# Optimization experiments

Measured on AMD Instinct MI355X. Metric: run time of the kernel, lower is better.

## Reference

```python
import jax, jax.numpy as jnp
import numpy as np

EPS = 1e-08
MARGIN = 0.5
B, D = 512, 768
N_CLASSES = 7


def setup_inputs() -> dict:
    key = jax.random.key(0)
    k1, k2 = jax.random.split(key)
    embeddings = jax.random.normal(k1, (B, D), dtype=jnp.float32)
    labels = jax.random.randint(k2, (B,), 0, N_CLASSES, dtype=jnp.int64)
    return {"embeddings": embeddings, "labels": labels}


def _cosine_distance_matrix(x):
    # 1 - x_i . x_j / (max(||x_i||, eps) * max(||x_j||, eps))  (torch cosine_similarity semantics)
    norms = jnp.maximum(jnp.linalg.norm(x, axis=-1, keepdims=True), EPS)
    xn = x / norms
    return 1.0 - xn @ xn.T  # (B, B)


def _triplet_mask(labels):
    n = labels.shape[0]
    ne = ~jnp.eye(n, dtype=bool)  # indices not equal
    distinct = ne[:, :, None] & ne[:, None, :] & ne[None, :, :]  # i!=j, i!=k, j!=k
    lbl_eq = labels[None, :] == labels[:, None]  # (B, B)
    valid = lbl_eq[:, :, None] & ~lbl_eq[:, None, :]  # label[i]==label[j], label[i]!=label[k]
    return distinct & valid


def reference(embeddings, labels):
    dist = _cosine_distance_matrix(embeddings)  # (B, B)
    # triplet_loss[i, j, k] = d(i, j) - d(i, k) + margin
    tl = dist[:, :, None] - dist[:, None, :] + MARGIN  # (B, B, B)
    mask = _triplet_mask(labels)
    tl = jax.nn.relu(tl * mask.astype(tl.dtype))
    num_pos = jnp.sum((tl > EPS).astype(jnp.float32))
    return jnp.sum(tl) / (num_pos + EPS)
```

## Files before the change

### kernel.cpp

```cpp
#include <hip/hip_runtime.h>


#define EPSF 1e-8f
#define MARGINF 0.5f
#define BN 512
#define DD 768
#define BT 64
#define SPLITK 8
#define KC (DD / SPLITK)
#define LPAD 104
#define NORMBLK 128

typedef __attribute__((ext_vector_type(8))) short bf16x8;
typedef __attribute__((ext_vector_type(4))) float f32x4;

__device__ __forceinline__ short f2bf(float f) {
    unsigned int u = __float_as_uint(f);
    return (short)((u + 0x7FFFu + ((u >> 16) & 1u)) >> 16);
}

__device__ __forceinline__ bf16x8 pack8(const float4& a, const float4& b) {
    bf16x8 r;
    r[0] = f2bf(a.x); r[1] = f2bf(a.y); r[2] = f2bf(a.z); r[3] = f2bf(a.w);
    r[4] = f2bf(b.x); r[5] = f2bf(b.y); r[6] = f2bf(b.z); r[7] = f2bf(b.w);
    return r;
}

__global__ __launch_bounds__(256) void prep_kernel(const float* __restrict__ x,
                                                   float* __restrict__ invn,
                                                   float* __restrict__ dotp) {
    int b = blockIdx.x;
    int t = threadIdx.x;
    int wv = t >> 6, lane = t & 63;

    if (b >= BN) {
        int row = (b - BN) * 4 + wv;
        float s = 0.f;
#pragma unroll
        for (int c = 0; c < 3; ++c) {
            float4 v = *(const float4*)&x[row * DD + (lane + c * 64) * 4];
            s += v.x * v.x + v.y * v.y + v.z * v.z + v.w * v.w;
        }
        for (int off = 32; off; off >>= 1) s += __shfl_down(s, off, 64);
        if (lane == 0) invn[row] = 1.0f / fmaxf(sqrtf(s), EPSF);
        return;
    }

    __shared__ __align__(16) short As[BT][LPAD];
    __shared__ __align__(16) short Bs[BT][LPAD];
    int bi = b & 7, bj = (b >> 3) & 7, bz = b >> 6;
    int i0 = bi * BT, j0 = bj * BT, kbase = bz * KC;

    {
        int row = t >> 2, fq = t & 3;
        const float* ap = &x[(i0 + row) * DD + kbase + fq * 8];
        const float* bp = &x[(j0 + row) * DD + kbase + fq * 8];
#pragma unroll
        for (int cc = 0; cc < 3; ++cc) {
            float4 a0 = *(const float4*)(ap + cc * 32);
            float4 a1 = *(const float4*)(ap + cc * 32 + 4);
            float4 b0 = *(const float4*)(bp + cc * 32);
            float4 b1 = *(const float4*)(bp + cc * 32 + 4);
            *(bf16x8*)&As[row][fq * 8 + cc * 32] = pack8(a0, a1);
            *(bf16x8*)&Bs[row][fq * 8 + cc * 32] = pack8(b0, b1);
        }
    }
    __syncthreads();

    int r16 = lane & 15;
    int kb8 = (lane >> 4) * 8;

    f32x4 accf[4];
#pragma unroll
    for (int c = 0; c < 4; ++c) accf[c] = (f32x4){0.f, 0.f, 0.f, 0.f};

#pragma unroll
    for (int s = 0; s < 3; ++s) {
        bf16x8 af = *(const bf16x8*)&As[wv * 16 + r16][kb8 + s * 32];
#pragma unroll
        for (int c = 0; c < 4; ++c) {
            bf16x8 bf_ = *(const bf16x8*)&Bs[c * 16 + r16][kb8 + s * 32];
            accf[c] = __builtin_amdgcn_mfma_f32_16x16x32_bf16(af, bf_, accf[c], 0, 0, 0);
        }
    }

    float* o = dotp + (size_t)bz * BN * BN;
    int crow = i0 + wv * 16 + (lane >> 4) * 4;
#pragma unroll
    for (int c = 0; c < 4; ++c) {
        int ccol = j0 + c * 16 + r16;
#pragma unroll
        for (int r = 0; r < 4; ++r)
            o[(crow + r) * BN + ccol] = accf[c][r];
    }
}

__global__ __launch_bounds__(256) void triplet_kernel(const float* __restrict__ dotp,
                                                      const float* __restrict__ invn,
                                                      const int* __restrict__ labels,
                                                      float* __restrict__ psum,
                                                      unsigned int* __restrict__ pcnt) {
    int r_ = blockIdx.x;
    int i = ((r_ & 7) << 6) | (r_ >> 3);
    int t = threadIdx.x;
    int w = t >> 6, lane = t & 63;
    __shared__ float drow[BN];
    __shared__ int lab[BN];
    __shared__ __align__(16) float dpos[528];
    __shared__ int wcnt[8];
    __shared__ int woff[9];
    __shared__ float redf[4];
    __shared__ unsigned int redc[4];

    lab[t] = labels[t];
    lab[t + 256] = labels[t + 256];
    float inv_i = invn[i];
#pragma unroll
    for (int e0 = 0; e0 < BN; e0 += 256) {
        int e = e0 + t;
        float s = 0.f;
#pragma unroll
        for (int z = 0; z < SPLITK; ++z) s += dotp[(size_t)z * BN * BN + i * BN + e];
        drow[e] = 1.0f - s * inv_i * invn[e];
    }
    __syncthreads();

    int li = lab[i];
    bool p0 = (lab[t] == li) && (t != i);
    bool p1 = (lab[t + 256] == li) && ((t + 256) != i);
    unsigned long long m0 = __ballot(p0);
    unsigned long long m1 = __ballot(p1);
    if (lane == 0) { wcnt[w] = __popcll(m0); wcnt[4 + w] = __popcll(m1); }
    __syncthreads();
    if (t == 0) {
        int s = 0;
#pragma unroll
        for (int q = 0; q < 8; ++q) { woff[q] = s; s += wcnt[q]; }
        woff[8] = s;
    }
    __syncthreads();
    unsigned long long lmask = (1ull << lane) - 1ull;
    if (p0) dpos[woff[w] + __popcll(m0 & lmask)] = drow[t] + MARGINF;
    if (p1) dpos[woff[4 + w] + __popcll(m1 & lmask)] = drow[t + 256] + MARGINF;
    int npos = woff[8];
    int npad = (npos + 15) & ~15;
    if (t < npad - npos) dpos[npos + t] = -1e30f;
    __syncthreads();

    float dk0 = (lab[t] != li) ? drow[t] : 1e30f;
    float dk1 = (lab[t + 256] != li) ? drow[t + 256] : 1e30f;
    float sum = 0.f;
    unsigned int cnt = 0;
    for (int n = 0; n < npad; n += 16) {
        float4 q[4];
#pragma unroll
        for (int v = 0; v < 4; ++v) q[v] = *(const float4*)&dpos[n + v * 4];
#pragma unroll
        for (int v = 0; v < 4; ++v) {
            float bv[4] = {q[v].x, q[v].y, q[v].z, q[v].w};
#pragma unroll
            for (int u = 0; u < 4; ++u) {
                float v0 = bv[u] - dk0;
                float v1 = bv[u] - dk1;
                sum += fmaxf(v0, 0.f);
                if (v0 > EPSF) cnt++;
                sum += fmaxf(v1, 0.f);
                if (v1 > EPSF) cnt++;
            }
        }
    }
    for (int off = 32; off; off >>= 1) {
        sum += __shfl_down(sum, off, 64);
        cnt += __shfl_down(cnt, off, 64);
    }
    if (lane == 0) { redf[w] = sum; redc[w] = cnt; }
    __syncthreads();
    if (t == 0) {
        psum[i] = redf[0] + redf[1] + redf[2] + redf[3];
        pcnt[i] = redc[0] + redc[1] + redc[2] + redc[3];
    }
}

__global__ __launch_bounds__(256) void reduce_kernel(const float* __restrict__ psum,
                                                     const unsigned int* __restrict__ pcnt,
                                                     float* __restrict__ out) {
    int t = threadIdx.x;
    double s = (double)psum[t] + (double)psum[t + 256];
    double c = (double)pcnt[t] + (double)pcnt[t + 256];
    for (int off = 32; off; off >>= 1) {
        s += __shfl_down(s, off, 64);
        c += __shfl_down(c, off, 64);
    }
    __shared__ double sred[4], cred[4];
    if ((t & 63) == 0) { sred[t >> 6] = s; cred[t >> 6] = c; }
    __syncthreads();
    if (t == 0) {
        double stot = sred[0] + sred[1] + sred[2] + sred[3];
        double ctot = cred[0] + cred[1] + cred[2] + cred[3];
        out[0] = (float)(stot / (ctot + 1e-8));
    }
}

extern "C" void kernel_launch(void* const* d_in, const int* in_sizes, int n_in,
                              void* d_out, int out_size, void* d_ws, size_t ws_size,
                              hipStream_t stream) {
    const float* x = (const float*)d_in[0];
    const int* labels = (const int*)d_in[1];
    float* out = (float*)d_out;

    char* ws = (char*)d_ws;
    float* invn = (float*)(ws + 256);
    float* psum = (float*)(ws + 4096);
    unsigned int* pcnt = (unsigned int*)(ws + 8192);
    float* dotp = (float*)(ws + 16384);

    prep_kernel<<<BN + NORMBLK, 256, 0, stream>>>(x, invn, dotp);
    triplet_kernel<<<BN, 256, 0, stream>>>(dotp, invn, labels, psum, pcnt);
    reduce_kernel<<<1, 256, 0, stream>>>(psum, pcnt, out);
}
```

Baseline: 17.64 us.

## Halve split-K partials and fuse final reduction into triplet kernel via atomics

Reduces the split-K factor from 8 to 4, so the GEMM runs half as many blocks with twice the K per block and the triplet kernel reads half as many partial dot-product planes, now with float2 loads. The separate reduce kernel is dropped: each triplet block atomically adds its sum and count into one of 64 striped slots, and the last block, found through an atomic counter, does the final division. A memset is added to zero the counters and slots each call. This trades one kernel launch and part of the partial-buffer traffic for a memset launch, atomic contention, and less parallelism in the GEMM.

```diff
diff --git a/kernel.cpp b/kernel.cpp
--- a/kernel.cpp
+++ b/kernel.cpp
@@ -6,9 +6,10 @@
 #define BN 512
 #define DD 768
 #define BT 64
-#define SPLITK 8
+#define SPLITK 4
 #define KC (DD / SPLITK)
-#define LPAD 104
+#define LPAD 200
+#define GBLK 256
 #define NORMBLK 128
 
 typedef __attribute__((ext_vector_type(8))) short bf16x8;
@@ -33,8 +34,8 @@
     int t = threadIdx.x;
     int wv = t >> 6, lane = t & 63;
 
-    if (b >= BN) {
-        int row = (b - BN) * 4 + wv;
+    if (b >= GBLK) {
+        int row = (b - GBLK) * 4 + wv;
         float s = 0.f;
 #pragma unroll
         for (int c = 0; c < 3; ++c) {
@@ -56,7 +57,7 @@
         const float* ap = &x[(i0 + row) * DD + kbase + fq * 8];
         const float* bp = &x[(j0 + row) * DD + kbase + fq * 8];
 #pragma unroll
-        for (int cc = 0; cc < 3; ++cc) {
+        for (int cc = 0; cc < 6; ++cc) {
             float4 a0 = *(const float4*)(ap + cc * 32);
             float4 a1 = *(const float4*)(ap + cc * 32 + 4);
             float4 b0 = *(const float4*)(bp + cc * 32);
@@ -75,7 +76,7 @@
     for (int c = 0; c < 4; ++c) accf[c] = (f32x4){0.f, 0.f, 0.f, 0.f};
 
 #pragma unroll
-    for (int s = 0; s < 3; ++s) {
+    for (int s = 0; s < 6; ++s) {
         bf16x8 af = *(const bf16x8*)&As[wv * 16 + r16][kb8 + s * 32];
 #pragma unroll
         for (int c = 0; c < 4; ++c) {
@@ -98,8 +99,9 @@
 __global__ __launch_bounds__(256) void triplet_kernel(const float* __restrict__ dotp,
                                                       const float* __restrict__ invn,
                                                       const int* __restrict__ labels,
-                                                      float* __restrict__ psum,
-                                                      unsigned int* __restrict__ pcnt) {
+                                                      char* __restrict__ accb,
+                                                      unsigned int* __restrict__ ctr,
+                                                      float* __restrict__ out) {
     int r_ = blockIdx.x;
     int i = ((r_ & 7) << 6) | (r_ >> 3);
     int t = threadIdx.x;
@@ -111,17 +113,22 @@
     __shared__ int woff[9];
     __shared__ float redf[4];
     __shared__ unsigned int redc[4];
-
+    __shared__ unsigned int lastflag;
+
+    if (t == 0) lastflag = 0u;
     lab[t] = labels[t];
     lab[t + 256] = labels[t + 256];
     float inv_i = invn[i];
-#pragma unroll
-    for (int e0 = 0; e0 < BN; e0 += 256) {
-        int e = e0 + t;
-        float s = 0.f;
-#pragma unroll
-        for (int z = 0; z < SPLITK; ++z) s += dotp[(size_t)z * BN * BN + i * BN + e];
-        drow[e] = 1.0f - s * inv_i * invn[e];
+    {
+        float2 iv = *(const float2*)&invn[2 * t];
+        float s0 = 0.f, s1 = 0.f;
+#pragma unroll
+        for (int z = 0; z < SPLITK; ++z) {
+            float2 p = *(const float2*)&dotp[(size_t)z * BN * BN + i * BN + 2 * t];
+            s0 += p.x; s1 += p.y;
+        }
+        drow[2 * t]     = 1.0f - s0 * inv_i * iv.x;
+        drow[2 * t + 1] = 1.0f - s1 * inv_i * iv.y;
     }
     __syncthreads();
 
@@ -176,28 +183,27 @@
     if (lane == 0) { redf[w] = sum; redc[w] = cnt; }
     __syncthreads();
     if (t == 0) {
-        psum[i] = redf[0] + redf[1] + redf[2] + redf[3];
-        pcnt[i] = redc[0] + redc[1] + redc[2] + redc[3];
-    }
-}
-
-__global__ __launch_bounds__(256) void reduce_kernel(const float* __restrict__ psum,
-                                                     const unsigned int* __restrict__ pcnt,
-                                                     float* __restrict__ out) {
-    int t = threadIdx.x;
-    double s = (double)psum[t] + (double)psum[t + 256];
-    double c = (double)pcnt[t] + (double)pcnt[t + 256];
-    for (int off = 32; off; off >>= 1) {
-        s += __shfl_down(s, off, 64);
-        c += __shfl_down(c, off, 64);
-    }
-    __shared__ double sred[4], cred[4];
-    if ((t & 63) == 0) { sred[t >> 6] = s; cred[t >> 6] = c; }
-    __syncthreads();
-    if (t == 0) {
-        double stot = sred[0] + sred[1] + sred[2] + sred[3];
-        double ctot = cred[0] + cred[1] + cred[2] + cred[3];
-        out[0] = (float)(stot / (ctot + 1e-8));
+        float stot = redf[0] + redf[1] + redf[2] + redf[3];
+        unsigned int ctot = redc[0] + redc[1] + redc[2] + redc[3];
+        double* dslot = (double*)(accb + (size_t)(i & 63) * 64);
+        unsigned int* cslot = (unsigned int*)(accb + (size_t)(i & 63) * 64 + 8);
+        atomicAdd(dslot, (double)stot);
+        atomicAdd(cslot, ctot);
+        __threadfence();
+        unsigned int old = atomicAdd(ctr, 1u);
+        if (old == BN - 1) lastflag = 1u;
+    }
+    __syncthreads();
+    if (lastflag && t < 64) {
+        __threadfence();
+        double s = atomicAdd((double*)(accb + (size_t)t * 64), 0.0);
+        unsigned int c = atomicAdd((unsigned int*)(accb + (size_t)t * 64 + 8), 0u);
+        double cs = (double)c;
+        for (int off = 32; off; off >>= 1) {
+            s += __shfl_down(s, off, 64);
+            cs += __shfl_down(cs, off, 64);
+        }
+        if (t == 0) out[0] = (float)(s / (cs + 1e-8));
     }
 }
 
@@ -209,12 +215,12 @@
     float* out = (float*)d_out;
 
     char* ws = (char*)d_ws;
-    float* invn = (float*)(ws + 256);
-    float* psum = (float*)(ws + 4096);
-    unsigned int* pcnt = (unsigned int*)(ws + 8192);
+    unsigned int* ctr = (unsigned int*)(ws + 64);
+    char* accb = ws + 4096;
+    float* invn = (float*)(ws + 8192);
     float* dotp = (float*)(ws + 16384);
 
-    prep_kernel<<<BN + NORMBLK, 256, 0, stream>>>(x, invn, dotp);
-    triplet_kernel<<<BN, 256, 0, stream>>>(dotp, invn, labels, psum, pcnt);
-    reduce_kernel<<<1, 256, 0, stream>>>(psum, pcnt, out);
-}
+    hipMemsetAsync(ws, 0, 8192, stream);
+    prep_kernel<<<GBLK + NORMBLK, 256, 0, stream>>>(x, invn, dotp);
+    triplet_kernel<<<BN, 256, 0, stream>>>(dotp, invn, labels, accb, ctr, out);
+}
```

New measurement: 27.83 us. 1.58x slower.
